# Performance work log

Measured on AMD Instinct MI355X. Metric: run time of the kernel, lower is better.

## Reference

```python
import jax, jax.numpy as jnp
import numpy as np

N_EMBD = 1024
HIDDEN = 4 * N_EMBD          # 4096
ADAPT = HIDDEN // 16         # 256
NUM_EXPERTS = 8
B, S = 4, 2048
LN_EPS = 1e-5


def setup_inputs() -> dict:
    key = jax.random.key(0)
    ks = jax.random.split(key, 8)
    x = jax.random.normal(ks[0], (B, S, N_EMBD), dtype=jnp.float32)
    # top-1 routing: one-hot expert weights (disjoint masks, standard MoE dispatch)
    route = jax.random.randint(ks[1], (B, S), 0, NUM_EXPERTS)
    expert_weights = jax.nn.one_hot(route, NUM_EXPERTS, dtype=jnp.float32)
    up_scale = 0.1 / N_EMBD ** 0.5
    adapt_scale0 = 0.1 / HIDDEN ** 0.5
    adapt_scale = 0.01 / ADAPT ** 0.5
    W_up = jax.random.normal(ks[2], (HIDDEN, N_EMBD), dtype=jnp.float32) * up_scale
    W_adapt = jax.random.normal(ks[3], (ADAPT, HIDDEN), dtype=jnp.float32) * adapt_scale0
    W_exp_adapters = jax.random.normal(ks[4], (NUM_EXPERTS, ADAPT, ADAPT), dtype=jnp.float32) * adapt_scale
    ln_gamma = jnp.ones((NUM_EXPERTS, ADAPT), dtype=jnp.float32)
    ln_beta = jnp.zeros((NUM_EXPERTS, ADAPT), dtype=jnp.float32)
    W_expert_proj = jax.random.normal(ks[5], (HIDDEN, ADAPT), dtype=jnp.float32) * adapt_scale
    W_out = jax.random.normal(ks[6], (N_EMBD, HIDDEN), dtype=jnp.float32) * adapt_scale
    return {"x": x, "expert_weights": expert_weights, "W_up": W_up,
            "W_adapt": W_adapt, "W_exp_adapters": W_exp_adapters,
            "ln_gamma": ln_gamma, "ln_beta": ln_beta,
            "W_expert_proj": W_expert_proj, "W_out": W_out}


def reference(x, expert_weights, W_up, W_adapt, W_exp_adapters, ln_gamma, ln_beta, W_expert_proj, W_out):
    b, s, d = x.shape
    T = b * s
    E = expert_weights.shape[-1]
    xt = x.reshape(T, d)

    # shared MLP path (silu(up_proj(x))) -> output_proj
    h = jax.nn.silu(xt @ W_up.T)                      # [T, HIDDEN]
    shared_out = (h @ W_out.T).reshape(b, s, d)       # [B, S, D]

    active = expert_weights.reshape(T, E) > 0         # [T, E]
    any_active = jnp.any(active, axis=-1)             # [T]
    last_idx = E - 1 - jnp.argmax(active[:, ::-1], axis=-1)  # [T]

    # pre_adapt (silu(up) recomputed == h) -> adapt_proj
    a = h @ W_adapt.T                                 # [T, ADAPT]
    # per-expert adapter linears, then select the winning expert per token
    a_all = jnp.einsum('td,eod->teo', a, W_exp_adapters)      # [T, E, ADAPT]
    a_sel = jnp.take_along_axis(a_all, last_idx[:, None, None], axis=1)[:, 0]  # [T, ADAPT]

    # per-expert LayerNorm params gathered per token
    g = ln_gamma[last_idx]                            # [T, ADAPT]
    be = ln_beta[last_idx]
    mu = jnp.mean(a_sel, axis=-1, keepdims=True)
    var = jnp.mean(jnp.square(a_sel - mu), axis=-1, keepdims=True)
    a_norm = (a_sel - mu) * jax.lax.rsqrt(var + LN_EPS) * g + be

    h2 = a_norm @ W_expert_proj.T                     # [T, HIDDEN]
    e_out = h2 @ W_out.T                              # [T, D]
    combined = jnp.where(any_active[:, None], e_out, 0.0).reshape(b, s, d)
    return shared_out + 0.1 * combined
```

## Files before the change

### kernel.cpp

```cpp
#include <hip/hip_runtime.h>
#include <cstdint>

#define TOK  8192
#define DEMB 1024
#define HID  4096
#define ADP  256
#define NEXP 8
#define KAUG 4352

typedef __bf16 bf16x8 __attribute__((ext_vector_type(8)));
typedef float  f32x4  __attribute__((ext_vector_type(4)));

__device__ __forceinline__ unsigned short f2bf(float f) {
  unsigned int u = __float_as_uint(f);
  u += 0x7fffu + ((u >> 16) & 1u);
  return (unsigned short)(u >> 16);
}
__device__ __forceinline__ float bf2f(unsigned short b) {
  return __uint_as_float(((unsigned int)b) << 16);
}

__global__ __launch_bounds__(256) void convert_a(
    const float* __restrict__ x, const float* __restrict__ wup,
    const float* __restrict__ ew,
    unsigned short* __restrict__ xb, unsigned short* __restrict__ wub,
    int* __restrict__ route) {
  int b = blockIdx.x;
  if (b >= 6144) {
    int t = (b - 6144) * 256 + threadIdx.x;
    const float* p = ew + (size_t)t * NEXP;
    int r = -1;
#pragma unroll
    for (int e = 0; e < NEXP; ++e)
      if (p[e] > 0.f) r = e;
    route[t] = r;
    return;
  }
  const float* src; unsigned short* dst; int lb;
  if (b < 4096) { src = x;   dst = xb;  lb = b; }
  else          { src = wup; dst = wub; lb = b - 4096; }
  size_t base = (size_t)lb * 2048;
#pragma unroll
  for (int h = 0; h < 2; ++h) {
    size_t off = base + (size_t)h * 1024 + (size_t)threadIdx.x * 4;
    float4 v = *(const float4*)(src + off);
    ushort4 o;
    o.x = f2bf(v.x); o.y = f2bf(v.y); o.z = f2bf(v.z); o.w = f2bf(v.w);
    *(ushort4*)(dst + off) = o;
  }
}

__device__ __forceinline__ void remap_xcd(int li, int gx, int gy,
                                          int& bx, int& by) {
  int xcd = li & 7;
  int slot = li >> 3;
  bx = slot % gx;
  by = xcd * (gy >> 3) + slot / gx;
}

#define PHASE_MID()                                       \
  __builtin_amdgcn_s_barrier();                           \
  asm volatile("s_waitcnt lgkmcnt(0)" ::: "memory");      \
  __builtin_amdgcn_sched_barrier(0);                      \
  __builtin_amdgcn_s_setprio(1)

#define PHASE_END()                                       \
  __builtin_amdgcn_s_setprio(0);                          \
  __builtin_amdgcn_sched_barrier(0);                      \
  __builtin_amdgcn_s_barrier()

#define PHASE_END_VM(N)                                   \
  __builtin_amdgcn_s_setprio(0);                          \
  __builtin_amdgcn_sched_barrier(0);                      \
  asm volatile("s_waitcnt vmcnt(" #N ")" ::: "memory");   \
  __builtin_amdgcn_s_barrier()

__device__ __forceinline__ void stage_tile(const unsigned short* __restrict__ g,
                                           int ldg, unsigned short* lds,
                                           int wave, int lane) {
  int srow = lane >> 3;
  int scol = ((lane & 7) ^ (srow & 7)) * 8;
#pragma unroll
  for (int c = 0; c < 4; ++c) {
    int chunk = wave * 4 + c;
    const unsigned short* gp = g + (size_t)(chunk * 8 + srow) * ldg + scol;
    unsigned short* lp = lds + chunk * 512;
    __builtin_amdgcn_global_load_lds(
        (const __attribute__((address_space(1))) unsigned int*)(uintptr_t)gp,
        (__attribute__((address_space(3))) unsigned int*)(uintptr_t)lp,
        16, 0, 0);
  }
}

template <int EPI>
__device__ __forceinline__ void gemm_body(
    int bxr, int byr, int bz,
    const unsigned short* __restrict__ A, int lda,
    const unsigned short* __restrict__ B, int ldb,
    void* __restrict__ C, int ldc, int kLen, long splitStride,
    unsigned short* As, unsigned short* Bs) {
  const int lane = threadIdx.x & 63;
  const int wave = threadIdx.x >> 6;
  const int wm = wave >> 1, wn = wave & 1;
  const long rowBase = (long)byr * 128;
  const long colBase = (long)bxr * 128;
  const int ks = bz * kLen;
  const unsigned short* Ap = A + rowBase * lda + ks;
  const unsigned short* Bp = B + colBase * ldb + ks;
  f32x4 acc[4][4] = {};

  for (int kt = 0; kt < kLen; kt += 64) {
    stage_tile(Ap + kt, lda, As, wave, lane);
    stage_tile(Bp + kt, ldb, Bs, wave, lane);
    __syncthreads();
#pragma unroll
    for (int kk = 0; kk < 64; kk += 32) {
      const int kb = (kk >> 3) + (lane >> 4);
      const int sw = kb ^ (lane & 7);
      bf16x8 af[4], bfr[4];
#pragma unroll
      for (int mt = 0; mt < 4; ++mt) {
        int m = wm * 64 + mt * 16 + (lane & 15);
        af[mt] = *(const bf16x8*)&As[m * 64 + sw * 8];
      }
#pragma unroll
      for (int nt = 0; nt < 4; ++nt) {
        int n = wn * 64 + nt * 16 + (lane & 15);
        bfr[nt] = *(const bf16x8*)&Bs[n * 64 + sw * 8];
      }
#pragma unroll
      for (int mt = 0; mt < 4; ++mt)
#pragma unroll
        for (int nt = 0; nt < 4; ++nt)
          acc[mt][nt] = __builtin_amdgcn_mfma_f32_16x16x32_bf16(
              af[mt], bfr[nt], acc[mt][nt], 0, 0, 0);
    }
    __syncthreads();
  }

  const int rsub = (lane >> 4) * 4;
  const int csub = lane & 15;
#pragma unroll
  for (int mt = 0; mt < 4; ++mt) {
#pragma unroll
    for (int nt = 0; nt < 4; ++nt) {
      long col = colBase + wn * 64 + nt * 16 + csub;
#pragma unroll
      for (int r = 0; r < 4; ++r) {
        long row = rowBase + wm * 64 + mt * 16 + rsub + r;
        float v = acc[mt][nt][r];
        if (EPI == 0) {
          float s = __fdividef(v, 1.0f + __expf(-v));
          ((unsigned short*)C)[row * ldc + col] = f2bf(s);
        } else {
          ((float*)C + splitStride * bz)[row * ldc + col] = v;
        }
      }
    }
  }
}

__global__ __launch_bounds__(256, 3) void fused2(
    const unsigned short* __restrict__ xb, const unsigned short* __restrict__ wub,
    unsigned short* __restrict__ haug,
    const float* __restrict__ wout, const float* __restrict__ wadapt,
    const float* __restrict__ wexp, const float* __restrict__ wp,
    unsigned short* __restrict__ wob, unsigned short* __restrict__ wab,
    unsigned short* __restrict__ web, unsigned short* __restrict__ wpT) {
  __shared__ char smem[32768];
  int li = blockIdx.x;
  if (li < 2048) {
    int bx, by;
    remap_xcd(li, 32, 64, bx, by);
    gemm_body<0>(bx, by, 0, xb, DEMB, wub, DEMB, haug, KAUG, DEMB, 0,
                 (unsigned short*)smem, (unsigned short*)(smem + 16384));
    return;
  }
  int cb = li - 2048;
  if (cb < 2816) {
    const float* src; unsigned short* dst; int lb; bool strided = false;
    if (cb < 2048)      { src = wout;   dst = wob; lb = cb;        strided = true; }
    else if (cb < 2560) { src = wadapt; dst = wab; lb = cb - 2048; }
    else                { src = wexp;   dst = web; lb = cb - 2560; }
    size_t base = (size_t)lb * 2048;
#pragma unroll
    for (int h = 0; h < 2; ++h) {
      size_t off = base + (size_t)h * 1024 + (size_t)threadIdx.x * 4;
      float4 v = *(const float4*)(src + off);
      ushort4 o;
      o.x = f2bf(v.x); o.y = f2bf(v.y); o.z = f2bf(v.z); o.w = f2bf(v.w);
      size_t doff = strided ? (off >> 12) * KAUG + (off & 4095) : off;
      *(ushort4*)(dst + doff) = o;
    }
    return;
  }
  float (*tile)[65] = (float(*)[65])smem;
  int wli = cb - 2816;
  const int h0 = (wli & 63) * 64;
  const int a0 = (wli >> 6) * 64;
  const int t = threadIdx.x;
  const int r = t >> 4;
  const int c = (t & 15) * 4;
#pragma unroll
  for (int p = 0; p < 4; ++p) {
    int row = p * 16 + r;
    float4 v = *(const float4*)(wp + (size_t)(h0 + row) * ADP + a0 + c);
    tile[c + 0][row] = v.x;
    tile[c + 1][row] = v.y;
    tile[c + 2][row] = v.z;
    tile[c + 3][row] = v.w;
  }
  __syncthreads();
#pragma unroll
  for (int q = 0; q < 2; ++q) {
    int idx = q * 256 + t;
    int al = idx >> 3;
    int hg = (idx & 7) * 8;
    unsigned int w0 = (unsigned int)f2bf(tile[al][hg + 0]) |
                      ((unsigned int)f2bf(tile[al][hg + 1]) << 16);
    unsigned int w1 = (unsigned int)f2bf(tile[al][hg + 2]) |
                      ((unsigned int)f2bf(tile[al][hg + 3]) << 16);
    unsigned int w2 = (unsigned int)f2bf(tile[al][hg + 4]) |
                      ((unsigned int)f2bf(tile[al][hg + 5]) << 16);
    unsigned int w3 = (unsigned int)f2bf(tile[al][hg + 6]) |
                      ((unsigned int)f2bf(tile[al][hg + 7]) << 16);
    *(uint4*)(wpT + (size_t)(a0 + al) * HID + h0 + hg) =
        make_uint4(w0, w1, w2, w3);
  }
}

__global__ __launch_bounds__(512, 4) void gemm_n256(
    const unsigned short* __restrict__ A0, int lda0,
    const unsigned short* __restrict__ B0, int ldb0,
    float* __restrict__ C0, int kLen0, long ss0, int nb0,
    const unsigned short* __restrict__ A1, int lda1,
    const unsigned short* __restrict__ B1, int ldb1,
    float* __restrict__ C1, int kLen1, long ss1) {
  __shared__ unsigned short As[128 * 64];
  __shared__ unsigned short Bs[256 * 64];
  const int lane = threadIdx.x & 63;
  const int wave = threadIdx.x >> 6;
  const int wm = wave >> 2, wn = wave & 3;
  int li = blockIdx.x;
  const unsigned short *A, *B;
  float* C;
  int lda, ldb, kLen, bz;
  long ss, rowBase;
  if (li < nb0) {
    bz = li >> 6;
    int bx, by;
    remap_xcd(li & 63, 1, 64, bx, by);
    A = A0; lda = lda0; B = B0; ldb = ldb0; C = C0; kLen = kLen0; ss = ss0;
    rowBase = (long)by * 128;
  } else {
    int wli = li - nb0;
    bz = wli >> 3;
    A = A1; lda = lda1; B = B1; ldb = ldb1; C = C1; kLen = kLen1; ss = ss1;
    rowBase = (long)(wli & 7) * 128;
  }
  const unsigned short* Ap = A + rowBase * lda + (size_t)bz * kLen;
  const unsigned short* Bp = B + (size_t)bz * kLen;
  const int srow = lane >> 3;
  const int scol = ((lane & 7) ^ (srow & 7)) * 8;
  f32x4 acc[4][4] = {};

  for (int kt = 0; kt < kLen; kt += 64) {
#pragma unroll
    for (int c = 0; c < 2; ++c) {
      int chunk = wave * 2 + c;
      __builtin_amdgcn_global_load_lds(
          (const __attribute__((address_space(1))) unsigned int*)(uintptr_t)(
              Ap + (size_t)(chunk * 8 + srow) * lda + kt + scol),
          (__attribute__((address_space(3))) unsigned int*)(uintptr_t)(
              As + chunk * 512),
          16, 0, 0);
    }
#pragma unroll
    for (int c = 0; c < 4; ++c) {
      int chunk = wave * 4 + c;
      __builtin_amdgcn_global_load_lds(
          (const __attribute__((address_space(1))) unsigned int*)(uintptr_t)(
              Bp + (size_t)(chunk * 8 + srow) * ldb + kt + scol),
          (__attribute__((address_space(3))) unsigned int*)(uintptr_t)(
              Bs + chunk * 512),
          16, 0, 0);
    }
    __syncthreads();
#pragma unroll
    for (int kk = 0; kk < 64; kk += 32) {
      const int kb = (kk >> 3) + (lane >> 4);
      const int sw = kb ^ (lane & 7);
      bf16x8 af[4], bfr[4];
#pragma unroll
      for (int mt = 0; mt < 4; ++mt) {
        int m = wm * 64 + mt * 16 + (lane & 15);
        af[mt] = *(const bf16x8*)&As[m * 64 + sw * 8];
      }
#pragma unroll
      for (int nt = 0; nt < 4; ++nt) {
        int n = wn * 64 + nt * 16 + (lane & 15);
        bfr[nt] = *(const bf16x8*)&Bs[n * 64 + sw * 8];
      }
#pragma unroll
      for (int mt = 0; mt < 4; ++mt)
#pragma unroll
        for (int nt = 0; nt < 4; ++nt)
          acc[mt][nt] = __builtin_amdgcn_mfma_f32_16x16x32_bf16(
              af[mt], bfr[nt], acc[mt][nt], 0, 0, 0);
    }
    __syncthreads();
  }

  const int rsub = (lane >> 4) * 4;
  const int csub = lane & 15;
  float* Cz = C + ss * bz;
#pragma unroll
  for (int mt = 0; mt < 4; ++mt) {
#pragma unroll
    for (int nt = 0; nt < 4; ++nt) {
      long col = wn * 64 + nt * 16 + csub;
#pragma unroll
      for (int r = 0; r < 4; ++r) {
        long row = rowBase + wm * 64 + mt * 16 + rsub + r;
        Cz[row * ADP + col] = acc[mt][nt][r];
      }
    }
  }
}

__device__ __forceinline__ void read_frag4(const unsigned short* base, int lane,
                                           int rowoff, int kk, bf16x8* dst) {
#pragma unroll
  for (int i = 0; i < 4; ++i) {
    int rr = rowoff + i * 16 + (lane & 15);
    int sw = ((kk >> 3) + (lane >> 4)) ^ (lane & 7);
    dst[i] = *(const bf16x8*)&base[rr * 64 + sw * 8];
  }
}

template <int NH>
__device__ __forceinline__ void mfma8(const bf16x8* af, const bf16x8* bf,
                                      f32x4 acc[4][4]) {
#pragma unroll
  for (int mt = 0; mt < 4; ++mt)
#pragma unroll
    for (int q = 0; q < 2; ++q)
      acc[mt][NH * 2 + q] = __builtin_amdgcn_mfma_f32_16x16x32_bf16(
          af[mt], bf[NH * 2 + q], acc[mt][NH * 2 + q], 0, 0, 0);
}

__global__ __launch_bounds__(512, 2) void gemm8p(
    const unsigned short* __restrict__ A, int lda,
    const unsigned short* __restrict__ B, int ldb,
    float* __restrict__ C, int ldc, int kLen) {
  __shared__ unsigned short As[2][128 * 64];
  __shared__ unsigned short Bs[2][256 * 64];
  const int lane = threadIdx.x & 63;
  const int wave = threadIdx.x >> 6;
  const int wm = wave >> 2, wn = wave & 3;
  int li = blockIdx.x + gridDim.x * blockIdx.y;
  int bx, by;
  remap_xcd(li, gridDim.x, gridDim.y, bx, by);
  const long rowBase = (long)by * 128;
  const long colBase = (long)bx * 256;
  const int srow = lane >> 3;
  const int scol = ((lane & 7) ^ (srow & 7)) * 8;
  const unsigned short* Ag = A + (rowBase + srow) * (long)lda + scol;
  const unsigned short* Bg = B + (colBase + srow) * (long)ldb + scol;
  const int NT = kLen >> 6;

  auto stA = [&](int buf, int t) {
#pragma unroll
    for (int c = 0; c < 2; ++c) {
      int chunk = wave * 2 + c;
      __builtin_amdgcn_global_load_lds(
          (const __attribute__((address_space(1))) unsigned int*)(uintptr_t)(
              Ag + (size_t)chunk * 8 * lda + (size_t)t * 64),
          (__attribute__((address_space(3))) unsigned int*)(uintptr_t)(
              &As[buf][chunk * 512]),
          16, 0, 0);
    }
  };
  auto stB = [&](int buf, int t, int h) {
#pragma unroll
    for (int c = 0; c < 2; ++c) {
      int chunk = h * 16 + wave * 2 + c;
      __builtin_amdgcn_global_load_lds(
          (const __attribute__((address_space(1))) unsigned int*)(uintptr_t)(
              Bg + (size_t)chunk * 8 * ldb + (size_t)t * 64),
          (__attribute__((address_space(3))) unsigned int*)(uintptr_t)(
              &Bs[buf][chunk * 512]),
          16, 0, 0);
    }
  };

  f32x4 acc[4][4] = {};
  bf16x8 af0[4], af1[4], bf0[4], bf1[4];

  stB(0, 0, 0);
  stB(0, 0, 1);
  stA(0, 0);
  if (NT > 1) {
    stA(1, 1);
    stB(1, 1, 0);
    asm volatile("s_waitcnt vmcnt(4)" ::: "memory");
  } else {
    asm volatile("s_waitcnt vmcnt(0)" ::: "memory");
  }
  __builtin_amdgcn_s_barrier();
  read_frag4(&As[0][0], lane, wm * 64, 0, af0);

  for (int t = 0; t < NT; ++t) {
    const int b = t & 1;
    read_frag4(&Bs[b][0], lane, wn * 64, 0, bf0);
    if (t + 1 < NT) stB(b ^ 1, t + 1, 1);
    PHASE_MID();
    mfma8<0>(af0, bf0, acc);
    PHASE_END();
    read_frag4(&As[b][0], lane, wm * 64, 32, af1);
    PHASE_MID();
    mfma8<1>(af0, bf0, acc);
    PHASE_END();
    read_frag4(&Bs[b][0], lane, wn * 64, 32, bf1);
    PHASE_MID();
    mfma8<0>(af1, bf1, acc);
    PHASE_END_VM(4);
    if (t + 1 < NT) read_frag4(&As[b ^ 1][0], lane, wm * 64, 0, af0);
    if (t + 2 < NT) { stA(b, t + 2); stB(b, t + 2, 0); }
    PHASE_MID();
    mfma8<1>(af1, bf1, acc);
    PHASE_END_VM(4);
  }

  const int rsub = (lane >> 4) * 4;
  const int csub = lane & 15;
#pragma unroll
  for (int mt = 0; mt < 4; ++mt) {
#pragma unroll
    for (int nt = 0; nt < 4; ++nt) {
      long col = colBase + wn * 64 + nt * 16 + csub;
#pragma unroll
      for (int r = 0; r < 4; ++r) {
        long row = rowBase + wm * 64 + mt * 16 + rsub + r;
        C[row * ldc + col] = acc[mt][nt][r];
      }
    }
  }
}

__global__ __launch_bounds__(256) void reduce_both(
    const float* __restrict__ P, unsigned short* __restrict__ ab,
    const float* __restrict__ Pw, unsigned short* __restrict__ wob) {
  int b = blockIdx.x;
  if (b < 2048) {
    size_t i = ((size_t)b * 256 + threadIdx.x) * 4;
    const size_t stride = (size_t)TOK * ADP;
    float4 p0 = *(const float4*)(P + i);
    float4 p1 = *(const float4*)(P + stride + i);
    float4 p2 = *(const float4*)(P + 2 * stride + i);
    float4 p3 = *(const float4*)(P + 3 * stride + i);
    ushort4 o;
    o.x = f2bf(p0.x + p1.x + p2.x + p3.x);
    o.y = f2bf(p0.y + p1.y + p2.y + p3.y);
    o.z = f2bf(p0.z + p1.z + p2.z + p3.z);
    o.w = f2bf(p0.w + p1.w + p2.w + p3.w);
    *(ushort4*)(ab + i) = o;
  } else {
    size_t i = ((size_t)(b - 2048) * 256 + threadIdx.x) * 4;
    const size_t stride = (size_t)DEMB * ADP;
    float4 s = *(const float4*)(Pw + i);
#pragma unroll
    for (int k = 1; k < 8; ++k) {
      float4 p = *(const float4*)(Pw + k * stride + i);
      s.x += p.x; s.y += p.y; s.z += p.z; s.w += p.w;
    }
    size_t d = i >> 8, a = i & 255;
    ushort4 o;
    o.x = f2bf(0.1f * s.x); o.y = f2bf(0.1f * s.y);
    o.z = f2bf(0.1f * s.z); o.w = f2bf(0.1f * s.w);
    *(ushort4*)(wob + d * KAUG + HID + a) = o;
  }
}

__global__ __launch_bounds__(512, 4) void gemm_exp_ln(
    const unsigned short* __restrict__ A,
    const unsigned short* __restrict__ Wexp,
    const int* __restrict__ route,
    const float* __restrict__ gamma, const float* __restrict__ beta,
    unsigned short* __restrict__ haug) {
  __shared__ unsigned short As[128 * 64];
  __shared__ unsigned short Bs[256 * 64];
  __shared__ float red1[4][128];
  __shared__ float red2[4][128];
  const int lane = threadIdx.x & 63;
  const int wave = threadIdx.x >> 6;
  const int wm = wave >> 2, wn = wave & 3;
  int li = blockIdx.x + gridDim.x * blockIdx.y;
  int bx, by;
  remap_xcd(li, gridDim.x, gridDim.y, bx, by);
  const long rowBase = (long)by * 128;
  const unsigned short* Ap = A + rowBase * ADP;
  const unsigned short* Bp = Wexp + (size_t)bx * ADP * ADP;
  const int srow = lane >> 3;
  const int scol = ((lane & 7) ^ (srow & 7)) * 8;
  f32x4 acc[4][4] = {};

  for (int kt = 0; kt < ADP; kt += 64) {
#pragma unroll
    for (int c = 0; c < 2; ++c) {
      int chunk = wave * 2 + c;
      __builtin_amdgcn_global_load_lds(
          (const __attribute__((address_space(1))) unsigned int*)(uintptr_t)(
              Ap + (size_t)(chunk * 8 + srow) * ADP + kt + scol),
          (__attribute__((address_space(3))) unsigned int*)(uintptr_t)(
              As + chunk * 512),
          16, 0, 0);
    }
#pragma unroll
    for (int c = 0; c < 4; ++c) {
      int chunk = wave * 4 + c;
      __builtin_amdgcn_global_load_lds(
          (const __attribute__((address_space(1))) unsigned int*)(uintptr_t)(
              Bp + (size_t)(chunk * 8 + srow) * ADP + kt + scol),
          (__attribute__((address_space(3))) unsigned int*)(uintptr_t)(
              Bs + chunk * 512),
          16, 0, 0);
    }
    __syncthreads();
#pragma unroll
    for (int kk = 0; kk < 64; kk += 32) {
      const int kb = (kk >> 3) + (lane >> 4);
      const int sw = kb ^ (lane & 7);
      bf16x8 af[4], bfr[4];
#pragma unroll
      for (int mt = 0; mt < 4; ++mt) {
        int m = wm * 64 + mt * 16 + (lane & 15);
        af[mt] = *(const bf16x8*)&As[m * 64 + sw * 8];
      }
#pragma unroll
      for (int nt = 0; nt < 4; ++nt) {
        int n = wn * 64 + nt * 16 + (lane & 15);
        bfr[nt] = *(const bf16x8*)&Bs[n * 64 + sw * 8];
      }
#pragma unroll
      for (int mt = 0; mt < 4; ++mt)
#pragma unroll
        for (int nt = 0; nt < 4; ++nt)
          acc[mt][nt] = __builtin_amdgcn_mfma_f32_16x16x32_bf16(
              af[mt], bfr[nt], acc[mt][nt], 0, 0, 0);
    }
    __syncthreads();
  }

  float ls1[4][4], ls2[4][4];
#pragma unroll
  for (int mt = 0; mt < 4; ++mt)
#pragma unroll
    for (int r = 0; r < 4; ++r) {
      float s1 = 0.f, s2 = 0.f;
#pragma unroll
      for (int nt = 0; nt < 4; ++nt) {
        float v = acc[mt][nt][r];
        s1 += v; s2 += v * v;
      }
      ls1[mt][r] = s1; ls2[mt][r] = s2;
    }
#pragma unroll
  for (int m = 1; m < 16; m <<= 1)
#pragma unroll
    for (int mt = 0; mt < 4; ++mt)
#pragma unroll
      for (int r = 0; r < 4; ++r) {
        ls1[mt][r] += __shfl_xor(ls1[mt][r], m);
        ls2[mt][r] += __shfl_xor(ls2[mt][r], m);
      }
  if ((lane & 15) == 0) {
    int g = lane >> 4;
#pragma unroll
    for (int mt = 0; mt < 4; ++mt)
#pragma unroll
      for (int r = 0; r < 4; ++r) {
        int rl = wm * 64 + mt * 16 + g * 4 + r;
        red1[wn][rl] = ls1[mt][r];
        red2[wn][rl] = ls2[mt][r];
      }
  }
  __syncthreads();
  const int rsub = (lane >> 4) * 4;
  const int csub = lane & 15;
  float gv[4], bv[4];
#pragma unroll
  for (int nt = 0; nt < 4; ++nt) {
    int col = wn * 64 + nt * 16 + csub;
    gv[nt] = gamma[bx * ADP + col];
    bv[nt] = beta[bx * ADP + col];
  }
#pragma unroll
  for (int mt = 0; mt < 4; ++mt) {
#pragma unroll
    for (int r = 0; r < 4; ++r) {
      int rl = wm * 64 + mt * 16 + rsub + r;
      long row = rowBase + rl;
      if (route[row] != bx) continue;
      float t1 = red1[0][rl] + red1[1][rl] + red1[2][rl] + red1[3][rl];
      float t2 = red2[0][rl] + red2[1][rl] + red2[2][rl] + red2[3][rl];
      float mu = t1 * (1.0f / ADP);
      float var = t2 * (1.0f / ADP) - mu * mu;
      float rstd = rsqrtf(var + 1e-5f);
#pragma unroll
      for (int nt = 0; nt < 4; ++nt) {
        int col = wn * 64 + nt * 16 + csub;
        float val = (acc[mt][nt][r] - mu) * rstd * gv[nt] + bv[nt];
        haug[row * KAUG + HID + col] = f2bf(val);
      }
    }
  }
}

extern "C" void kernel_launch(void* const* d_in, const int* in_sizes, int n_in,
                              void* d_out, int out_size, void* d_ws, size_t ws_size,
                              hipStream_t stream) {
  const float* x     = (const float*)d_in[0];
  const float* ew    = (const float*)d_in[1];
  const float* W_up  = (const float*)d_in[2];
  const float* W_ad  = (const float*)d_in[3];
  const float* W_ex  = (const float*)d_in[4];
  const float* gam   = (const float*)d_in[5];
  const float* bet   = (const float*)d_in[6];
  const float* W_pr  = (const float*)d_in[7];
  const float* W_out = (const float*)d_in[8];
  float* out = (float*)d_out;

  char* ws = (char*)d_ws;
  size_t off = 0;
  auto alloc = [&](size_t n) {
    char* p = ws + off;
    off += (n + 255) & ~(size_t)255;
    return p;
  };
  unsigned short* xb   = (unsigned short*)alloc((size_t)TOK * DEMB * 2);
  unsigned short* wub  = (unsigned short*)alloc((size_t)HID * DEMB * 2);
  unsigned short* wob  = (unsigned short*)alloc((size_t)DEMB * KAUG * 2);
  unsigned short* wab  = (unsigned short*)alloc((size_t)ADP * HID * 2);
  unsigned short* web  = (unsigned short*)alloc((size_t)NEXP * ADP * ADP * 2);
  unsigned short* wpT  = (unsigned short*)alloc((size_t)ADP * HID * 2);
  unsigned short* Haug = (unsigned short*)alloc((size_t)TOK * KAUG * 2);
  float*          P    = (float*)alloc((size_t)4 * TOK * ADP * 4);
  float*          Pw   = (float*)alloc((size_t)8 * DEMB * ADP * 4);
  unsigned short* ab   = (unsigned short*)alloc((size_t)TOK * ADP * 2);
  int*          route  = (int*)alloc((size_t)TOK * 4);

  convert_a<<<6176, 256, 0, stream>>>(x, W_up, ew, xb, wub, route);
  fused2<<<5120, 256, 0, stream>>>(xb, wub, Haug, W_out, W_ad, W_ex, W_pr,
                                   wob, wab, web, wpT);
  gemm_n256<<<320, 512, 0, stream>>>(
      Haug, KAUG, wab, HID, P, HID / 4, (long)TOK * ADP, 256,
      wob, KAUG, wpT, HID, Pw, HID / 8, (long)DEMB * ADP);
  reduce_both<<<2304, 256, 0, stream>>>(P, ab, Pw, wob);
  gemm_exp_ln<<<dim3(NEXP, TOK / 128), 512, 0, stream>>>(
      ab, web, route, gam, bet, Haug);
  gemm8p<<<dim3(DEMB / 256, TOK / 128), 512, 0, stream>>>(
      Haug, KAUG, wob, KAUG, out, DEMB, KAUG);
}
```

Before: 336.0 us.

## Shrink final GEMM tile to 128x128 with two-phase pipeline and higher occupancy

The final output GEMM moves from 128x256 tiles to 128x128 tiles, doubling the grid to 512 blocks and allowing 4 blocks per CU through launch bounds. The k-loop is restructured from four MFMA phases to two, with new load/wait ordering. The LayerNorm statistics reduction in the expert GEMM is also rewritten to shuffle per row inline instead of through staged arrays, to cut register pressure. Smaller tiles lower arithmetic intensity and raise global/L2 traffic for the B operand, in exchange for better CU fill and latency hiding.

```diff
diff --git a/kernel.cpp b/kernel.cpp
--- a/kernel.cpp
+++ b/kernel.cpp
@@ -63,11 +63,6 @@
   asm volatile("s_waitcnt lgkmcnt(0)" ::: "memory");      \
   __builtin_amdgcn_sched_barrier(0);                      \
   __builtin_amdgcn_s_setprio(1)
-
-#define PHASE_END()                                       \
-  __builtin_amdgcn_s_setprio(0);                          \
-  __builtin_amdgcn_sched_barrier(0);                      \
-  __builtin_amdgcn_s_barrier()
 
 #define PHASE_END_VM(N)                                   \
   __builtin_amdgcn_s_setprio(0);                          \
@@ -338,23 +333,22 @@
   }
 }
 
-template <int NH>
-__device__ __forceinline__ void mfma8(const bf16x8* af, const bf16x8* bf,
-                                      f32x4 acc[4][4]) {
-#pragma unroll
-  for (int mt = 0; mt < 4; ++mt)
-#pragma unroll
-    for (int q = 0; q < 2; ++q)
-      acc[mt][NH * 2 + q] = __builtin_amdgcn_mfma_f32_16x16x32_bf16(
-          af[mt], bf[NH * 2 + q], acc[mt][NH * 2 + q], 0, 0, 0);
-}
-
-__global__ __launch_bounds__(512, 2) void gemm8p(
+__device__ __forceinline__ void read_frag2(const unsigned short* base, int lane,
+                                           int rowoff, int kk, bf16x8* dst) {
+#pragma unroll
+  for (int i = 0; i < 2; ++i) {
+    int rr = rowoff + i * 16 + (lane & 15);
+    int sw = ((kk >> 3) + (lane >> 4)) ^ (lane & 7);
+    dst[i] = *(const bf16x8*)&base[rr * 64 + sw * 8];
+  }
+}
+
+__global__ __launch_bounds__(512, 4) void gemm8h(
     const unsigned short* __restrict__ A, int lda,
     const unsigned short* __restrict__ B, int ldb,
     float* __restrict__ C, int ldc, int kLen) {
   __shared__ unsigned short As[2][128 * 64];
-  __shared__ unsigned short Bs[2][256 * 64];
+  __shared__ unsigned short Bs[2][128 * 64];
   const int lane = threadIdx.x & 63;
   const int wave = threadIdx.x >> 6;
   const int wm = wave >> 2, wn = wave & 3;
@@ -362,48 +356,46 @@
   int bx, by;
   remap_xcd(li, gridDim.x, gridDim.y, bx, by);
   const long rowBase = (long)by * 128;
-  const long colBase = (long)bx * 256;
+  const long colBase = (long)bx * 128;
   const int srow = lane >> 3;
   const int scol = ((lane & 7) ^ (srow & 7)) * 8;
   const unsigned short* Ag = A + (rowBase + srow) * (long)lda + scol;
   const unsigned short* Bg = B + (colBase + srow) * (long)ldb + scol;
   const int NT = kLen >> 6;
 
-  auto stA = [&](int buf, int t) {
+  auto st = [&](unsigned short* lds, const unsigned short* g, int t) {
 #pragma unroll
     for (int c = 0; c < 2; ++c) {
       int chunk = wave * 2 + c;
       __builtin_amdgcn_global_load_lds(
           (const __attribute__((address_space(1))) unsigned int*)(uintptr_t)(
-              Ag + (size_t)chunk * 8 * lda + (size_t)t * 64),
+              g + (size_t)chunk * 8 * lda + (size_t)t * 64),
           (__attribute__((address_space(3))) unsigned int*)(uintptr_t)(
-              &As[buf][chunk * 512]),
+              lds + chunk * 512),
           16, 0, 0);
     }
   };
-  auto stB = [&](int buf, int t, int h) {
+  auto stB2 = [&](unsigned short* lds, int t) {
 #pragma unroll
     for (int c = 0; c < 2; ++c) {
-      int chunk = h * 16 + wave * 2 + c;
+      int chunk = wave * 2 + c;
       __builtin_amdgcn_global_load_lds(
           (const __attribute__((address_space(1))) unsigned int*)(uintptr_t)(
               Bg + (size_t)chunk * 8 * ldb + (size_t)t * 64),
           (__attribute__((address_space(3))) unsigned int*)(uintptr_t)(
-              &Bs[buf][chunk * 512]),
+              lds + chunk * 512),
           16, 0, 0);
     }
   };
 
-  f32x4 acc[4][4] = {};
-  bf16x8 af0[4], af1[4], bf0[4], bf1[4];
-
-  stB(0, 0, 0);
-  stB(0, 0, 1);
-  stA(0, 0);
+  f32x4 acc[4][2] = {};
+  bf16x8 af0[4], af1[4], bf0[2], bf1[2];
+
+  stB2(Bs[0], 0);
+  st(As[0], Ag, 0);
   if (NT > 1) {
-    stA(1, 1);
-    stB(1, 1, 0);
-    asm volatile("s_waitcnt vmcnt(4)" ::: "memory");
+    st(As[1], Ag, 1);
+    asm volatile("s_waitcnt vmcnt(2)" ::: "memory");
   } else {
     asm volatile("s_waitcnt vmcnt(0)" ::: "memory");
   }
@@ -412,24 +404,28 @@
 
   for (int t = 0; t < NT; ++t) {
     const int b = t & 1;
-    read_frag4(&Bs[b][0], lane, wn * 64, 0, bf0);
-    if (t + 1 < NT) stB(b ^ 1, t + 1, 1);
+    read_frag2(&Bs[b][0], lane, wn * 32, 0, bf0);
+    read_frag4(&As[b][0], lane, wm * 64, 32, af1);
+    if (t + 1 < NT) stB2(Bs[b ^ 1], t + 1);
     PHASE_MID();
-    mfma8<0>(af0, bf0, acc);
-    PHASE_END();
-    read_frag4(&As[b][0], lane, wm * 64, 32, af1);
+#pragma unroll
+    for (int mt = 0; mt < 4; ++mt)
+#pragma unroll
+      for (int nt = 0; nt < 2; ++nt)
+        acc[mt][nt] = __builtin_amdgcn_mfma_f32_16x16x32_bf16(
+            af0[mt], bf0[nt], acc[mt][nt], 0, 0, 0);
+    if (t + 1 < NT) { PHASE_END_VM(2); } else { PHASE_END_VM(0); }
+    read_frag2(&Bs[b][0], lane, wn * 32, 32, bf1);
+    if (t + 1 < NT) read_frag4(&As[b ^ 1][0], lane, wm * 64, 0, af0);
+    if (t + 2 < NT) st(As[b], Ag, t + 2);
     PHASE_MID();
-    mfma8<1>(af0, bf0, acc);
-    PHASE_END();
-    read_frag4(&Bs[b][0], lane, wn * 64, 32, bf1);
-    PHASE_MID();
-    mfma8<0>(af1, bf1, acc);
-    PHASE_END_VM(4);
-    if (t + 1 < NT) read_frag4(&As[b ^ 1][0], lane, wm * 64, 0, af0);
-    if (t + 2 < NT) { stA(b, t + 2); stB(b, t + 2, 0); }
-    PHASE_MID();
-    mfma8<1>(af1, bf1, acc);
-    PHASE_END_VM(4);
+#pragma unroll
+    for (int mt = 0; mt < 4; ++mt)
+#pragma unroll
+      for (int nt = 0; nt < 2; ++nt)
+        acc[mt][nt] = __builtin_amdgcn_mfma_f32_16x16x32_bf16(
+            af1[mt], bf1[nt], acc[mt][nt], 0, 0, 0);
+    if (t + 2 < NT) { PHASE_END_VM(2); } else { PHASE_END_VM(0); }
   }
 
   const int rsub = (lane >> 4) * 4;
@@ -437,8 +433,8 @@
 #pragma unroll
   for (int mt = 0; mt < 4; ++mt) {
 #pragma unroll
-    for (int nt = 0; nt < 4; ++nt) {
-      long col = colBase + wn * 64 + nt * 16 + csub;
+    for (int nt = 0; nt < 2; ++nt) {
+      long col = colBase + wn * 32 + nt * 16 + csub;
 #pragma unroll
       for (int r = 0; r < 4; ++r) {
         long row = rowBase + wm * 64 + mt * 16 + rsub + r;
@@ -552,9 +548,8 @@
     __syncthreads();
   }
 
-  float ls1[4][4], ls2[4][4];
-#pragma unroll
-  for (int mt = 0; mt < 4; ++mt)
+#pragma unroll
+  for (int mt = 0; mt < 4; ++mt) {
 #pragma unroll
     for (int r = 0; r < 4; ++r) {
       float s1 = 0.f, s2 = 0.f;
@@ -563,27 +558,17 @@
         float v = acc[mt][nt][r];
         s1 += v; s2 += v * v;
       }
-      ls1[mt][r] = s1; ls2[mt][r] = s2;
-    }
-#pragma unroll
-  for (int m = 1; m < 16; m <<= 1)
-#pragma unroll
-    for (int mt = 0; mt < 4; ++mt)
-#pragma unroll
-      for (int r = 0; r < 4; ++r) {
-        ls1[mt][r] += __shfl_xor(ls1[mt][r], m);
-        ls2[mt][r] += __shfl_xor(ls2[mt][r], m);
-      }
-  if ((lane & 15) == 0) {
-    int g = lane >> 4;
-#pragma unroll
-    for (int mt = 0; mt < 4; ++mt)
-#pragma unroll
-      for (int r = 0; r < 4; ++r) {
-        int rl = wm * 64 + mt * 16 + g * 4 + r;
-        red1[wn][rl] = ls1[mt][r];
-        red2[wn][rl] = ls2[mt][r];
-      }
+#pragma unroll
+      for (int m = 1; m < 16; m <<= 1) {
+        s1 += __shfl_xor(s1, m);
+        s2 += __shfl_xor(s2, m);
+      }
+      if ((lane & 15) == 0) {
+        int rl = wm * 64 + mt * 16 + (lane >> 4) * 4 + r;
+        red1[wn][rl] = s1;
+        red2[wn][rl] = s2;
+      }
+    }
   }
   __syncthreads();
   const int rsub = (lane >> 4) * 4;
@@ -659,6 +644,6 @@
   reduce_both<<<2304, 256, 0, stream>>>(P, ab, Pw, wob);
   gemm_exp_ln<<<dim3(NEXP, TOK / 128), 512, 0, stream>>>(
       ab, web, route, gam, bet, Haug);
-  gemm8p<<<dim3(DEMB / 256, TOK / 128), 512, 0, stream>>>(
+  gemm8h<<<dim3(DEMB / 128, TOK / 128), 512, 0, stream>>>(
       Haug, KAUG, wob, KAUG, out, DEMB, KAUG);
 }
```

New measurement: 325.9 us. -3.0%, faster.
